# Optimization experiments

Measured on AMD Instinct MI355X. Metric: run time of the kernel, lower is better.

Reference implementation:

```python
import jax, jax.numpy as jnp
import numpy as np

B, S, D = 1, 2048, 3072
H, DH = 24, 128
ENC, NIP = 512, 64
COND = (512 // 8) * (512 // 8) * 16 // 64  # 1024 cond tokens per lora
RANK, ALPHA, LW, IP_SCALE = 16, 16.0, 1.0, 1.0
EPS = 1e-5


def _rms(x):
    return x * jax.lax.rsqrt(jnp.mean(x * x, axis=-1, keepdims=True) + EPS)


def _to_heads(x):
    b, s, _ = x.shape
    return x.reshape(b, s, H, DH).transpose(0, 2, 1, 3)  # [B,H,S,DH]


def _from_heads(x):
    b, h, s, d = x.shape
    return x.transpose(0, 2, 1, 3).reshape(b, s, h * d)


def _lora(x, dn, up):
    # token mask keeps only the cond block (number=0, n_loras=1 -> last COND tokens)
    y = ((x[:, -COND:, :] @ dn) @ up) * (ALPHA / RANK)
    z = jnp.zeros((x.shape[0], x.shape[1] - COND, up.shape[1]), x.dtype)
    return jnp.concatenate([z, y], axis=1)


def _sdpa(q, k, v, mask=None):
    s = jnp.einsum('bhqd,bhkd->bhqk', q, k) * (1.0 / np.sqrt(DH))
    if mask is not None:
        s = s + mask
    return jnp.einsum('bhqk,bhkd->bhqd', jax.nn.softmax(s, axis=-1), v)


def _forward(hidden_states, encoder_hidden_states, image_emb,
             Wq, bq, Wk, bk, Wv, bv, Waq, baq, Wak, bak, Wav, bav,
             Wo, bo, Wao, bao, Wkip, Wvip,
             lq_dn, lq_up, lk_dn, lk_up, lv_dn, lv_up, lp_dn, lp_up):
    hs, ehs, img = hidden_states, encoder_hidden_states, image_emb
    # context (encoder) projections + RMSNorm on q/k
    eq = _rms(_to_heads(ehs @ Waq + baq))
    ek = _rms(_to_heads(ehs @ Wak + bak))
    ev = _to_heads(ehs @ Wav + bav)
    # main-stream q/k/v with masked LoRA branches
    q = hs @ Wq + bq + LW * _lora(hs, lq_dn, lq_up)
    k = hs @ Wk + bk + LW * _lora(hs, lk_dn, lk_up)
    v = hs @ Wv + bv + LW * _lora(hs, lv_dn, lv_up)
    q = _rms(_to_heads(q))
    k = _rms(_to_heads(k))
    v = _to_heads(v)
    # IP-adapter branch: extra K/V from image_emb, norm_added_k is RMSNorm(128)
    kip = _rms(_to_heads(img @ Wkip))
    vip = _to_heads(img @ Wvip)
    ip_out = _from_heads(_sdpa(q, kip, vip))  # [B,S,D]
    # concat encoder stream ahead of main stream
    q = jnp.concatenate([eq, q], axis=2)
    k = jnp.concatenate([ek, k], axis=2)
    v = jnp.concatenate([ev, v], axis=2)
    SL = ENC + S
    SB = SL - COND  # scaled_block_size
    m = jnp.ones((SL, SL), jnp.float32)
    m = m.at[:SB, :].set(0.0)        # non-cond rows attend everywhere
    m = m.at[SB:, SB:].set(0.0)      # single cond block attends to itself (n_loras=1)
    mask = m * (-1e20)
    out = _from_heads(_sdpa(q, k, v, mask))  # [B,SL,D]
    enc_out = out[:, :ENC, :]
    main = out[:, ENC:, :] + IP_SCALE * ip_out
    main = main @ Wo + bo
    main = main + LW * _lora(main, lp_dn, lp_up)  # proj LoRA (to_out dropout=identity)
    enc_out = enc_out @ Wao + bao
    return jnp.concatenate([enc_out, main], axis=1)  # [B, ENC+S, D]


def setup_inputs():
    key = jax.random.key(0)
    ks = iter(jax.random.split(key, 40))
    w = lambda *sh: jax.random.normal(next(ks), sh, jnp.float32) * 0.02
    return dict(
        hidden_states=jax.random.normal(next(ks), (B, S, D), jnp.float32),
        encoder_hidden_states=jax.random.normal(next(ks), (B, ENC, D), jnp.float32),
        image_emb=jax.random.normal(next(ks), (B, NIP, D), jnp.float32),
        Wq=w(D, D), bq=w(D), Wk=w(D, D), bk=w(D), Wv=w(D, D), bv=w(D),
        Waq=w(D, D), baq=w(D), Wak=w(D, D), bak=w(D), Wav=w(D, D), bav=w(D),
        Wo=w(D, D), bo=w(D), Wao=w(D, D), bao=w(D),
        Wkip=w(D, D), Wvip=w(D, D),
        lq_dn=w(D, RANK), lq_up=w(RANK, D), lk_dn=w(D, RANK), lk_up=w(RANK, D),
        lv_dn=w(D, RANK), lv_up=w(RANK, D), lp_dn=w(D, RANK), lp_up=w(RANK, D),
    )


def reference(hidden_states, encoder_hidden_states, image_emb,
              Wq, bq, Wk, bk, Wv, bv, Waq, baq, Wak, bak, Wav, bav,
              Wo, bo, Wao, bao, Wkip, Wvip,
              lq_dn, lq_up, lk_dn, lk_up, lv_dn, lv_up, lp_dn, lp_up):
    return _forward(hidden_states, encoder_hidden_states, image_emb,
                    Wq, bq, Wk, bk, Wv, bv, Waq, baq, Wak, bak, Wav, bav,
                    Wo, bo, Wao, bao, Wkip, Wvip,
                    lq_dn, lq_up, lk_dn, lk_up, lv_dn, lv_up, lp_dn, lp_up)
```

## Files before the change

kernel.cpp:

```cpp
#include <hip/hip_runtime.h>

typedef unsigned short u16;
typedef short s16x8 __attribute__((ext_vector_type(8)));
typedef float f32x4 __attribute__((ext_vector_type(4)));
typedef const __attribute__((address_space(1))) unsigned int* as1_u32p;
typedef __attribute__((address_space(3))) unsigned int* as3_u32p;

static_assert(sizeof(s16x8) == 16, "");

struct alignas(8) U16x4 { u16 x, y, z, w; };

__device__ __forceinline__ u16 f2bf(float f) {
  union { float f; unsigned u; } c; c.f = f;
  return (u16)((c.u + 0x7fffu + ((c.u >> 16) & 1u)) >> 16);
}
__device__ __forceinline__ float bf2f(u16 h) {
  union { unsigned u; float f; } c; c.u = ((unsigned)h) << 16;
  return c.f;
}
__device__ __forceinline__ void async16(const void* g, void* l) {
  __builtin_amdgcn_global_load_lds((as1_u32p)g, (as3_u32p)l, 16, 0, 0);
}

__launch_bounds__(256)
__global__ void lora_dn3(const float* __restrict__ X, int ldx,
                         const float* __restrict__ d0, const float* __restrict__ d1,
                         const float* __restrict__ d2, float* __restrict__ t) {
  __shared__ float red[4][48];
  const int m = blockIdx.x;
  const float* xr = X + (long)m * ldx;
  float p[48];
#pragma unroll
  for (int r = 0; r < 48; ++r) p[r] = 0.f;
  for (int k = threadIdx.x; k < 3072; k += 256) {
    float a = xr[k];
    const float* e0 = d0 + (long)k * 16;
    const float* e1 = d1 + (long)k * 16;
    const float* e2 = d2 + (long)k * 16;
#pragma unroll
    for (int r = 0; r < 16; ++r) {
      p[r]      += a * e0[r];
      p[16 + r] += a * e1[r];
      p[32 + r] += a * e2[r];
    }
  }
#pragma unroll
  for (int r = 0; r < 48; ++r)
#pragma unroll
    for (int st = 1; st < 64; st <<= 1) p[r] += __shfl_xor(p[r], st, 64);
  int lane = threadIdx.x & 63, w = threadIdx.x >> 6;
  if (lane == 0) {
#pragma unroll
    for (int r = 0; r < 48; ++r) red[w][r] = p[r];
  }
  __syncthreads();
  if (threadIdx.x < 48) {
    int r = threadIdx.x;
    t[(long)m * 48 + r] = red[0][r] + red[1][r] + red[2][r] + red[3][r];
  }
}

__launch_bounds__(256)
__global__ void wod_prep(const float* __restrict__ Wo, const float* __restrict__ bo,
                         const float* __restrict__ dn, float* __restrict__ Wod) {
  __shared__ float red[4][16];
  const int m = blockIdx.x;
  const float* xr = (m < 3072) ? Wo + (long)m * 3072 : bo;
  float p[16];
#pragma unroll
  for (int r = 0; r < 16; ++r) p[r] = 0.f;
  for (int k = threadIdx.x; k < 3072; k += 256) {
    float a = xr[k];
    const float* d = dn + (long)k * 16;
#pragma unroll
    for (int r = 0; r < 16; ++r) p[r] += a * d[r];
  }
#pragma unroll
  for (int r = 0; r < 16; ++r)
#pragma unroll
    for (int st = 1; st < 64; st <<= 1) p[r] += __shfl_xor(p[r], st, 64);
  int lane = threadIdx.x & 63, w = threadIdx.x >> 6;
  if (lane == 0) {
#pragma unroll
    for (int r = 0; r < 16; ++r) red[w][r] = p[r];
  }
  __syncthreads();
  if (threadIdx.x < 16) {
    int r = threadIdx.x;
    Wod[(long)m * 16 + r] = red[0][r] + red[1][r] + red[2][r] + red[3][r];
  }
}

__launch_bounds__(256)
__global__ void prep_all(const float* __restrict__ hs, const float* __restrict__ tl,
                         u16* __restrict__ hsb,
                         const float* __restrict__ ehs, u16* __restrict__ ehsb,
                         const float* __restrict__ img, u16* __restrict__ imgb,
                         const float* __restrict__ baq, const float* __restrict__ bak,
                         const float* __restrict__ bav, const float* __restrict__ bq,
                         const float* __restrict__ bk, const float* __restrict__ bv,
                         float* __restrict__ bpk,
                         const float* __restrict__ u0, const float* __restrict__ u1,
                         const float* __restrict__ u2, u16* __restrict__ WTbM) {
  const int b = blockIdx.x;
  if (b < 3136) {
    long idx = (long)b * 256 + threadIdx.x;
    long m = idx / 392, c = idx % 392;
    U16x4 o0, o1;
    if (c < 384) {
      const float* p = hs + m * 3072 + c * 8;
      float4 a = *(const float4*)p;
      float4 bb = *(const float4*)(p + 4);
      o0 = U16x4{f2bf(a.x), f2bf(a.y), f2bf(a.z), f2bf(a.w)};
      o1 = U16x4{f2bf(bb.x), f2bf(bb.y), f2bf(bb.z), f2bf(bb.w)};
    } else {
      u16 t[8];
#pragma unroll
      for (int i = 0; i < 8; ++i) {
        int r = (int)(c - 384) * 8 + i;
        float v = (m >= 1024 && r < 48) ? tl[(m - 1024) * 48 + r] : 0.f;
        t[i] = f2bf(v);
      }
      o0 = U16x4{t[0], t[1], t[2], t[3]};
      o1 = U16x4{t[4], t[5], t[6], t[7]};
    }
    u16* d = hsb + m * 3136 + c * 8;
    *(U16x4*)d = o0;
    *(U16x4*)(d + 4) = o1;
  } else if (b < 3904) {
    long i = ((long)(b - 3136) * 256 + threadIdx.x) * 8;
    float4 a = *(const float4*)(ehs + i);
    float4 bb = *(const float4*)(ehs + i + 4);
    *(U16x4*)(ehsb + i) = U16x4{f2bf(a.x), f2bf(a.y), f2bf(a.z), f2bf(a.w)};
    *(U16x4*)(ehsb + i + 4) = U16x4{f2bf(bb.x), f2bf(bb.y), f2bf(bb.z), f2bf(bb.w)};
  } else if (b < 4000) {
    long i = ((long)(b - 3904) * 256 + threadIdx.x) * 8;
    float4 a = *(const float4*)(img + i);
    float4 bb = *(const float4*)(img + i + 4);
    *(U16x4*)(imgb + i) = U16x4{f2bf(a.x), f2bf(a.y), f2bf(a.z), f2bf(a.w)};
    *(U16x4*)(imgb + i + 4) = U16x4{f2bf(bb.x), f2bf(bb.y), f2bf(bb.z), f2bf(bb.w)};
  } else if (b < 4072) {
    int i = (b - 4000) * 256 + threadIdx.x;
    if (i < 9216)
      bpk[i] = (i < 3072) ? baq[i] : (i < 6144) ? bak[i - 3072] : bav[i - 6144];
    else {
      int j = i - 9216;
      bpk[i] = (j < 3072) ? bq[j] : (j < 6144) ? bk[j - 3072] : bv[j - 6144];
    }
  } else {
    int idx = (b - 4072) * 256 + threadIdx.x;
    int n = idx >> 6, i = idx & 63;
    int seg = n / 3072;
    const float* up = (seg == 0) ? u0 : (seg == 1) ? u1 : u2;
    int r = i - seg * 16;
    float v = (r >= 0 && r < 16) ? up[(long)r * 3072 + (n - seg * 3072)] : 0.f;
    WTbM[(long)n * 3136 + 3072 + i] = f2bf(v);
  }
}

struct WT6 { const float* src[6]; u16* dst[6]; int ldd[6]; };

__launch_bounds__(256)
__global__ void transpose_w(WT6 args) {
  const float* src = args.src[blockIdx.z];
  u16* dst = args.dst[blockIdx.z];
  const int ldd = args.ldd[blockIdx.z];
  __shared__ float tile[32][33];
  int k0 = blockIdx.x * 32, n0 = blockIdx.y * 32;
  int r = threadIdx.x >> 3, c4 = (threadIdx.x & 7) * 4;
  float4 v = *(const float4*)(src + (long)(k0 + r) * 3072 + n0 + c4);
  tile[r][c4 + 0] = v.x; tile[r][c4 + 1] = v.y;
  tile[r][c4 + 2] = v.z; tile[r][c4 + 3] = v.w;
  __syncthreads();
  U16x4 o{f2bf(tile[c4 + 0][r]), f2bf(tile[c4 + 1][r]),
          f2bf(tile[c4 + 2][r]), f2bf(tile[c4 + 3][r])};
  *(U16x4*)(dst + (long)(n0 + r) * ldd + k0 + c4) = o;
}

__launch_bounds__(256)
__global__ void fill_wo_tail(const float* __restrict__ lp_up, u16* __restrict__ WTbM) {
  int idx = blockIdx.x * 256 + threadIdx.x;
  int n = idx >> 6, i = idx & 63;
  float v = (i < 16) ? lp_up[(long)i * 3072 + n] : 0.f;
  WTbM[(long)n * 3136 + 3072 + i] = f2bf(v);
}

__launch_bounds__(256)
__global__ void t_tail(u16* __restrict__ At, const float* __restrict__ Wod) {
  __shared__ float red[4][16];
  const int tok = blockIdx.x;
  u16* tail = At + (long)(512 + tok) * 3136 + 3072;
  if (tok < 1024) {
    if (threadIdx.x < 64) tail[threadIdx.x] = 0;
    return;
  }
  const u16* xr = At + (long)(512 + tok) * 3136;
  float p[16];
#pragma unroll
  for (int r = 0; r < 16; ++r) p[r] = 0.f;
  for (int n = threadIdx.x; n < 3072; n += 256) {
    float a = bf2f(xr[n]);
    const float* wd = Wod + (long)n * 16;
#pragma unroll
    for (int r = 0; r < 16; ++r) p[r] += a * wd[r];
  }
#pragma unroll
  for (int r = 0; r < 16; ++r)
#pragma unroll
    for (int st = 1; st < 64; st <<= 1) p[r] += __shfl_xor(p[r], st, 64);
  int lane = threadIdx.x & 63, w = threadIdx.x >> 6;
  if (lane == 0) {
#pragma unroll
    for (int r = 0; r < 16; ++r) red[w][r] = p[r];
  }
  __syncthreads();
  if (threadIdx.x < 64) {
    if (threadIdx.x < 16) {
      int r = threadIdx.x;
      float t = red[0][r] + red[1][r] + red[2][r] + red[3][r] + Wod[3072L * 16 + r];
      tail[r] = f2bf(t);
    } else {
      tail[threadIdx.x] = 0;
    }
  }
}

template <int BM, int MI, int NI>
__launch_bounds__(256)
__global__ void gemm_f32(const u16* __restrict__ A, int lda,
                         const u16* __restrict__ B, int ldb,
                         float* __restrict__ C, int ldc,
                         const float* __restrict__ bias, int KC, long cstride) {
  constexpr int WCOLS = 128 / (NI * 16);
  constexpr int ABYTES = BM * 128;
  __shared__ char smem[ABYTES + 128 * 128];
  char* As = smem;
  char* Bs = smem + ABYTES;
// ... 58 lines not shown
    for (int ni = 0; ni < NI; ++ni) {
      long col = n0 + wc * (NI * 16) + ni * 16 + lr;
      float bv = bias ? bias[col] : 0.f;
#pragma unroll
      for (int j = 0; j < 4; ++j) {
        long row = m0 + wr * (MI * 16) + mi * 16 + lg * 4 + j;
        C[row * ldc + col] = acc[mi][ni][j] + bv;
      }
    }
  }
}

__launch_bounds__(256)
__global__ void rms_ip(const float* __restrict__ in, u16* __restrict__ Ko,
                       u16* __restrict__ Vo) {
  const int t = blockIdx.x & 63;
  const int vhalf = blockIdx.x >> 6;
  const int col0 = vhalf ? 3072 : 0;
  u16* out = vhalf ? Vo : Ko;
  const int w = threadIdx.x >> 6, lane = threadIdx.x & 63;
  const long ps = 64LL * 6144;
#pragma unroll
  for (int hh = 0; hh < 6; ++hh) {
    int h = w * 6 + hh;
    const float* x = in + (long)t * 6144 + col0 + h * 128 + lane * 2;
    float a = x[0] + x[ps] + x[2 * ps] + x[3 * ps];
    float b = x[1] + x[1 + ps] + x[1 + 2 * ps] + x[1 + 3 * ps];
    float scale = 1.f;
    if (!vhalf) {
      float ss = a * a + b * b;
#pragma unroll
      for (int st = 1; st < 64; st <<= 1) ss += __shfl_xor(ss, st, 64);
      scale = rsqrtf(ss * (1.f / 128.f) + 1e-5f);
    }
    unsigned pa = f2bf(a * scale), pb = f2bf(b * scale);
    *(unsigned*)(out + ((long)h * 64 + t) * 128 + lane * 2) = pa | (pb << 16);
  }
}

__launch_bounds__(256)
__global__ void transpose_v(const u16* __restrict__ VB, u16* __restrict__ VT, int T) {
  __shared__ u16 tile[32][34];
  int h = blockIdx.z;
  int t0 = blockIdx.x * 32, d0 = blockIdx.y * 32;
  int r = threadIdx.x >> 3, c4 = (threadIdx.x & 7) * 4;
  U16x4 v = *(const U16x4*)(VB + ((long)h * T + t0 + r) * 128 + d0 + c4);
  tile[r][c4 + 0] = v.x; tile[r][c4 + 1] = v.y;
  tile[r][c4 + 2] = v.z; tile[r][c4 + 3] = v.w;
  __syncthreads();
  U16x4 o{tile[c4 + 0][r], tile[c4 + 1][r], tile[c4 + 2][r], tile[c4 + 3][r]};
  *(U16x4*)(VT + ((long)h * 128 + d0 + r) * T + t0 + c4) = o;
}

__launch_bounds__(256, 2)
__global__ void gemm_qkv(const u16* __restrict__ Aenc, const u16* __restrict__ Amain,
                         const u16* __restrict__ Benc, const u16* __restrict__ Bmain,
                         u16* __restrict__ Qo, u16* __restrict__ Ko, u16* __restrict__ VTo,
                         const float* __restrict__ bpk) {
  __shared__ char smem[49152];
  char* As = smem;
  char* Bs = smem + 16384;
  const int tid = threadIdx.x;
  const int w = tid >> 6, lane = tid & 63;
  const int lr = lane & 15, lg = lane >> 4;
  const int wr = w >> 1, wc = w & 1;
  const int flat = blockIdx.y * 20 + blockIdx.x;
  const int swz = (flat & 7) * 90 + (flat >> 3);
  const int mx = swz % 20;
  const long n0 = (long)(swz / 20) * 256;
  const u16* A;
  const u16* B;
  const float* bias;
  int lda, ldb, K, t0;
  long m0;
  if (mx < 4) {
    A = Aenc; lda = 3072; B = Benc; ldb = 3072; K = 3072; t0 = 0;
    m0 = (long)mx * 128; bias = bpk;
  } else {
    A = Amain; lda = 3136; B = Bmain; ldb = 3136; K = 3136; t0 = 512;
    m0 = (long)(mx - 4) * 128; bias = bpk + 9216;
  }
  f32x4 acc[4][8] = {};
  for (int kb = 0; kb < K; kb += 64) {
    __syncthreads();
#pragma unroll
    for (int i = 0; i < 4; ++i) {
      int x = (tid + 256 * i) * 16;
      int row = x >> 7;
      int sx = (x & 127) ^ ((row & 7) << 4);
      async16((const char*)(A + (m0 + row) * lda + kb) + sx, As + x);
    }
#pragma unroll
    for (int i = 0; i < 8; ++i) {
      int x = (tid + 256 * i) * 16;
      int row = x >> 7;
      int sx = (x & 127) ^ ((row & 7) << 4);
      async16((const char*)(B + (n0 + row) * ldb + kb) + sx, Bs + x);
    }
    __syncthreads();
#pragma unroll
    for (int kc = 0; kc < 2; ++kc) {
      s16x8 af[4], bfr[8];
#pragma unroll
      for (int mi = 0; mi < 4; ++mi) {
        int row = wr * 64 + mi * 16 + lr;
        af[mi] = *(const s16x8*)(As + (row << 7) + ((kc * 64 + lg * 16) ^ ((row & 7) << 4)));
      }
#pragma unroll
      for (int ni = 0; ni < 8; ++ni) {
        int row = wc * 128 + ni * 16 + lr;
        bfr[ni] = *(const s16x8*)(Bs + (row << 7) + ((kc * 64 + lg * 16) ^ ((row & 7) << 4)));
      }
#pragma unroll
      for (int mi = 0; mi < 4; ++mi)
#pragma unroll
        for (int ni = 0; ni < 8; ++ni)
          acc[mi][ni] = __builtin_amdgcn_mfma_f32_16x16x32_bf16(af[mi], bfr[ni], acc[mi][ni], 0, 0, 0);
    }
  }
  const int seg = (int)(n0 / 3072);
  const int head0 = (int)((n0 % 3072) >> 7);
#pragma unroll
  for (int ni = 0; ni < 8; ++ni) {
    float bv = bias[n0 + wc * 128 + ni * 16 + lr];
#pragma unroll
    for (int mi = 0; mi < 4; ++mi)
#pragma unroll
      for (int j = 0; j < 4; ++j) acc[mi][ni][j] += bv;
  }
  float scl[4][4];
  if (seg < 2) {
#pragma unroll
    for (int mi = 0; mi < 4; ++mi)
#pragma unroll
      for (int j = 0; j < 4; ++j) {
        float s = 0.f;
#pragma unroll
        for (int ni = 0; ni < 8; ++ni) s += acc[mi][ni][j] * acc[mi][ni][j];
#pragma unroll
        for (int st = 1; st < 16; st <<= 1) s += __shfl_xor(s, st, 16);
        scl[mi][j] = rsqrtf(s * (1.f / 128.f) + 1e-5f);
      }
  }
#pragma unroll
  for (int ph = 0; ph < 2; ++ph) {
    __syncthreads();
    if (wc == ph) {
      if (seg < 2) {
#pragma unroll
        for (int mi = 0; mi < 4; ++mi)
#pragma unroll
          for (int ni = 0; ni < 8; ++ni) {
            int d2 = (ni * 16 + lr) * 2;
#pragma unroll
            for (int j = 0; j < 4; ++j) {
              int tok = wr * 64 + mi * 16 + lg * 4 + j;
              *(u16*)(smem + tok * 256 + (d2 ^ ((tok & 7) << 4))) =
                  f2bf(acc[mi][ni][j] * scl[mi][j]);
            }
          }
      } else {
#pragma unroll
        for (int mi = 0; mi < 4; ++mi)
#pragma unroll
          for (int ni = 0; ni < 8; ++ni) {
            int d = ni * 16 + lr;
            int tok0b = (wr * 64 + mi * 16 + lg * 4) * 2;
            U16x4 o{f2bf(acc[mi][ni][0]), f2bf(acc[mi][ni][1]),
                    f2bf(acc[mi][ni][2]), f2bf(acc[mi][ni][3])};
            *(U16x4*)(smem + d * 256 + (tok0b ^ ((d & 7) << 4))) = o;
          }
      }
    }
    __syncthreads();
    const int headp = head0 + ph;
#pragma unroll
    for (int i = 0; i < 8; ++i) {
      int x = (tid + 256 * i) * 16;
      int row = x >> 8, col = x & 255;
      s16x8 vdat = *(const s16x8*)(smem + row * 256 + (col ^ ((row & 7) << 4)));
      if (seg < 2) {
        u16* g = (seg == 0 ? Qo : Ko) + ((long)headp * 2560 + t0 + m0 + row) * 128;
        *(s16x8*)((char*)g + col) = vdat;
      } else {
        u16* g = VTo + ((long)headp * 128 + row) * 2560 + t0 + m0;
        *(s16x8*)((char*)g + col) = vdat;
      }
    }
  }
}

__launch_bounds__(256)
__global__ void gemm_out(const u16* __restrict__ Atok, const u16* __restrict__ Benc,
                         const u16* __restrict__ Bmain, float* __restrict__ outp,
                         const float* __restrict__ bao, const float* __restrict__ bo) {
  __shared__ char smem[128 * 128 + 128 * 128];
  char* As = smem;
  char* Bs = smem + 128 * 128;
  const int tid = threadIdx.x;
  const int w = tid >> 6, lane = tid & 63;
  const int lr = lane & 15, lg = lane >> 4;
  const int wr = w >> 1, wc = w & 1;
  const int flat = blockIdx.y * 20 + blockIdx.x;
  const int swz = (flat & 7) * 60 + (flat >> 3);
  const int mx = swz % 20;
  const long n0 = (long)(swz / 20) * 128;
  const u16* A;
  const u16* B;
  const float* bias;
  float* C;
  int ldb, K;
  long m0;
  if (mx < 4) {
    A = Atok; B = Benc; ldb = 3072; K = 3072; bias = bao; C = outp;
    m0 = (long)mx * 128;
  } else {
    A = Atok + 512L * 3136; B = Bmain; ldb = 3136; K = 3136; bias = bo;
    C = outp + 512L * 3072; m0 = (long)(mx - 4) * 128;
  }
  f32x4 acc[4][4] = {};
  for (int kb = 0; kb < K; kb += 64) {
    __syncthreads();
#pragma unroll
    for (int i = 0; i < 4; ++i) {
      int x = (tid + 256 * i) * 16;
      int row = x >> 7;
      int sx = x ^ ((row & 7) << 4);
      async16((const char*)(A + (m0 + row) * 3136 + kb) + (sx & 127),
              As + ((w << 10) + (i << 12)));
    }
#pragma unroll
    for (int i = 0; i < 4; ++i) {
      int x = (tid + 256 * i) * 16;
      int row = x >> 7;
      int sx = x ^ ((row & 7) << 4);
      async16((const char*)(B + (n0 + row) * ldb + kb) + (sx & 127),
              Bs + ((w << 10) + (i << 12)));
    }
    __syncthreads();
#pragma unroll
    for (int kc = 0; kc < 2; ++kc) {
      s16x8 af[4], bfr[4];
#pragma unroll
      for (int mi = 0; mi < 4; ++mi) {
        int row = wr * 64 + mi * 16 + lr;
        int b = ((row << 7) + kc * 64 + lg * 16) ^ ((row & 7) << 4);
        af[mi] = *(const s16x8*)(As + b);
      }
#pragma unroll
      for (int ni = 0; ni < 4; ++ni) {
        int row = wc * 64 + ni * 16 + lr;
        int b = ((row << 7) + kc * 64 + lg * 16) ^ ((row & 7) << 4);
        bfr[ni] = *(const s16x8*)(Bs + b);
      }
#pragma unroll
      for (int mi = 0; mi < 4; ++mi)
#pragma unroll
        for (int ni = 0; ni < 4; ++ni)
          acc[mi][ni] = __builtin_amdgcn_mfma_f32_16x16x32_bf16(af[mi], bfr[ni], acc[mi][ni], 0, 0, 0);
    }
  }
#pragma unroll
  for (int mi = 0; mi < 4; ++mi) {
#pragma unroll
    for (int ni = 0; ni < 4; ++ni) {
      long col = n0 + wc * 64 + ni * 16 + lr;
      float bv = bias[col];
#pragma unroll
      for (int j = 0; j < 4; ++j) {
        long row = m0 + wr * 64 + mi * 16 + lg * 4 + j;
        C[row * 3072 + col] = acc[mi][ni][j] + bv;
      }
    }
  }
}

__launch_bounds__(512, 4)
__global__ void attn_fused(const u16* __restrict__ QB, const u16* __restrict__ KB,
                           const u16* __restrict__ VT, const u16* __restrict__ KipB,
                           const u16* __restrict__ VipT, u16* __restrict__ OutTok) {
  __shared__ char smem[81920];
  const int tid = threadIdx.x, w = tid >> 6, lane = tid & 63;
  const int lr = lane & 15, lg = lane >> 4;
  const int h = blockIdx.y;
  const int q0 = blockIdx.x * 128;
  const bool ip = (q0 >= 512);
  const u16* Qrow = QB + (long)(h * 2560 + q0 + w * 16 + lr) * 128;
  s16x8 qf[4];
#pragma unroll
  for (int dc = 0; dc < 4; ++dc) qf[dc] = *(const s16x8*)(Qrow + dc * 32 + lg * 8);
  f32x4 accO[8] = {};
  float l_r[4] = {0.f, 0.f, 0.f, 0.f};
  const int kv0 = (q0 >= 1536) ? 1536 : 0;
  const float sc = 0.08838834764831845f;

  auto stage_main = [&](int kv, int buf) {
#pragma unroll
    for (int i = 0; i < 2; ++i) {
      int x = (tid + 512 * i) * 16;
      int row = x >> 8;
      int sx = x ^ ((row & 7) << 4);
      async16((const char*)(KB + (long)(h * 2560 + kv + row) * 128) + (sx & 255),
              smem + buf * 16384 + ((i << 13) + (w << 10)));
    }
#pragma unroll
    for (int i = 0; i < 2; ++i) {
      int x = (tid + 512 * i) * 16;
      int row = x >> 7;
      int sx = x ^ ((row & 7) << 4);
      async16((const char*)(VT + (long)(h * 128 + row) * 2560 + kv) + (sx & 127),
              smem + 32768 + buf * 16384 + ((i << 13) + (w << 10)));
    }
  };
  auto stage_ip = [&](int buf) {
#pragma unroll
    for (int i = 0; i < 2; ++i) {
      int x = (tid + 512 * i) * 16;
      int row = x >> 8;
      int sx = x ^ ((row & 7) << 4);
      async16((const char*)(KipB + (long)(h * 64 + row) * 128) + (sx & 255),
              smem + buf * 16384 + ((i << 13) + (w << 10)));
    }
#pragma unroll
    for (int i = 0; i < 2; ++i) {
      int x = (tid + 512 * i) * 16;
      int row = x >> 7;
      int sx = x ^ ((row & 7) << 4);
      async16((const char*)(VipT + (long)(h * 128 + row) * 64) + (sx & 127),
              smem + 32768 + buf * 16384 + ((i << 13) + (w << 10)));
    }
  };

  stage_main(kv0, 0);
  __syncthreads();
  int cur = 0;
  for (int kv = kv0; kv < 2560; kv += 64) {
    if (kv + 64 < 2560) stage_main(kv + 64, cur ^ 1);
    else if (ip) stage_ip(cur ^ 1);
    const char* Ks = smem + cur * 16384;
    const char* Vs = smem + 32768 + cur * 16384;
    char* Pw = smem + 65536 + w * 2048;
    f32x4 s[4] = {};
#pragma unroll
    for (int kt = 0; kt < 4; ++kt)
#pragma unroll
      for (int dc = 0; dc < 4; ++dc) {
        int row = kt * 16 + lr;
        int b = ((row << 8) + dc * 64 + lg * 16) ^ ((row & 7) << 4);
        s16x8 kf = *(const s16x8*)(Ks + b);
        s[kt] = __builtin_amdgcn_mfma_f32_16x16x32_bf16(qf[dc], kf, s[kt], 0, 0, 0);
      }
#pragma unroll
    for (int kt = 0; kt < 4; ++kt)
#pragma unroll
      for (int j = 0; j < 4; ++j) {
        float pv = __expf(fmaf(s[kt][j], sc, -12.0f));
        l_r[j] += pv;
        int prow = lg * 4 + j;
        int b = ((prow << 7) + (kt * 16 + lr) * 2) ^ ((prow & 7) << 4);
        *(u16*)(Pw + b) = f2bf(pv);
      }
    asm volatile("s_waitcnt lgkmcnt(0)" ::: "memory");
#pragma unroll
    for (int kc = 0; kc < 2; ++kc) {
      int pb = ((lr << 7) + kc * 64 + lg * 16) ^ ((lr & 7) << 4);
      s16x8 pf = *(const s16x8*)(Pw + pb);
#pragma unroll
      for (int dt = 0; dt < 8; ++dt) {
        int row = dt * 16 + lr;
        int b = ((row << 7) + kc * 64 + lg * 16) ^ ((row & 7) << 4);
        s16x8 vf = *(const s16x8*)(Vs + b);
        accO[dt] = __builtin_amdgcn_mfma_f32_16x16x32_bf16(pf, vf, accO[dt], 0, 0, 0);
      }
    }
    __syncthreads();
    cur ^= 1;
  }
#pragma unroll
  for (int j = 0; j < 4; ++j) {
#pragma unroll
    for (int st = 1; st < 16; st <<= 1) l_r[j] += __shfl_xor(l_r[j], st, 16);
    l_r[j] = 1.f / l_r[j];
  }
#pragma unroll
  for (int dt = 0; dt < 8; ++dt)
#pragma unroll
    for (int j = 0; j < 4; ++j) accO[dt][j] *= l_r[j];
  if (ip) {
    const char* Ks = smem + cur * 16384;
    const char* Vs = smem + 32768 + cur * 16384;
    char* Pw = smem + 65536 + w * 2048;
    f32x4 s2[4] = {};
#pragma unroll
    for (int kt = 0; kt < 4; ++kt)
#pragma unroll
      for (int dc = 0; dc < 4; ++dc) {
        int row = kt * 16 + lr;
        int b = ((row << 8) + dc * 64 + lg * 16) ^ ((row & 7) << 4);
        s16x8 kf = *(const s16x8*)(Ks + b);
        s2[kt] = __builtin_amdgcn_mfma_f32_16x16x32_bf16(qf[dc], kf, s2[kt], 0, 0, 0);
      }
    float p2[4][4];
    float l2[4] = {0.f, 0.f, 0.f, 0.f};
#pragma unroll
    for (int kt = 0; kt < 4; ++kt)
#pragma unroll
      for (int j = 0; j < 4; ++j) {
        float pv = __expf(fmaf(s2[kt][j], sc, -12.0f));
        p2[kt][j] = pv;
        l2[j] += pv;
      }
#pragma unroll
    for (int j = 0; j < 4; ++j) {
#pragma unroll
      for (int st = 1; st < 16; st <<= 1) l2[j] += __shfl_xor(l2[j], st, 16);
      l2[j] = 1.f / l2[j];
    }
#pragma unroll
    for (int kt = 0; kt < 4; ++kt)
#pragma unroll
      for (int j = 0; j < 4; ++j) {
        int prow = lg * 4 + j;
        int b = ((prow << 7) + (kt * 16 + lr) * 2) ^ ((prow & 7) << 4);
        *(u16*)(Pw + b) = f2bf(p2[kt][j] * l2[j]);
      }
    asm volatile("s_waitcnt lgkmcnt(0)" ::: "memory");
#pragma unroll
// ... 25 lines not shown
                              void* d_out, int out_size, void* d_ws, size_t ws_size,
                              hipStream_t stream) {
  const float* hs    = (const float*)d_in[0];
  const float* ehs   = (const float*)d_in[1];
  const float* img   = (const float*)d_in[2];
  const float* Wq    = (const float*)d_in[3];
  const float* bq    = (const float*)d_in[4];
  const float* Wk    = (const float*)d_in[5];
  const float* bk    = (const float*)d_in[6];
  const float* Wv    = (const float*)d_in[7];
  const float* bv    = (const float*)d_in[8];
  const float* Waq   = (const float*)d_in[9];
  const float* baq   = (const float*)d_in[10];
  const float* Wak   = (const float*)d_in[11];
  const float* bak   = (const float*)d_in[12];
  const float* Wav   = (const float*)d_in[13];
  const float* bav   = (const float*)d_in[14];
  const float* Wo    = (const float*)d_in[15];
  const float* bo    = (const float*)d_in[16];
  const float* Wao   = (const float*)d_in[17];
  const float* bao   = (const float*)d_in[18];
  const float* Wkip  = (const float*)d_in[19];
  const float* Wvip  = (const float*)d_in[20];
  const float* lq_dn = (const float*)d_in[21];
  const float* lq_up = (const float*)d_in[22];
  const float* lk_dn = (const float*)d_in[23];
  const float* lk_up = (const float*)d_in[24];
  const float* lv_dn = (const float*)d_in[25];
  const float* lv_up = (const float*)d_in[26];
  const float* lp_dn = (const float*)d_in[27];
  const float* lp_up = (const float*)d_in[28];
  float* outp = (float*)d_out;

  char* ws = (char*)d_ws;
  size_t off = 0;
  auto take = [&](size_t b) { char* p = ws + off; off += (b + 255) & ~(size_t)255; return p; };
  u16*   WTbE = (u16*)take(3LL * 3072 * 3072 * 2);
  u16*   WTbM = (u16*)take(3LL * 3072 * 3136 * 2);
  u16*   hsb  = (u16*)take(2048LL * 3136 * 2);
  u16*   ehsb = (u16*)take(512LL * 3072 * 2);
  u16*   imgb = (u16*)take(64LL * 3072 * 2);
  u16*   VTf  = (u16*)take(24LL * 128 * 2560 * 2);
  float* IP0  = (float*)take(4LL * 64 * 6144 * 4);
  u16*   KipB = (u16*)take(24LL * 64 * 128 * 2);
  u16*   VipB = (u16*)take(24LL * 64 * 128 * 2);
  u16*   VipT = (u16*)take(24LL * 128 * 64 * 2);
  float* bpk  = (float*)take(2 * 9216 * 4);
  float* tl   = (float*)take(1024LL * 48 * 4);
  float* Wod  = (float*)take(3073LL * 16 * 4);
  u16* QBf = (u16*)d_out;
  u16* KBf = (u16*)d_out + 24LL * 2560 * 128;
  u16* AttnTok = hsb;
  u16* E1 = WTbE + 3072LL * 3072;

  lora_dn3<<<1024, 256, 0, stream>>>(hs + 1024LL * 3072, 3072, lq_dn, lk_dn, lv_dn, tl);
  prep_all<<<6376, 256, 0, stream>>>(hs, tl, hsb, ehs, ehsb, img, imgb,
                                     baq, bak, bav, bq, bk, bv, bpk,
                                     lq_up, lk_up, lv_up, WTbM);
  wod_prep<<<3073, 256, 0, stream>>>(Wo, bo, lp_dn, Wod);

  {
    WT6 a;
    a.src[0] = Waq; a.dst[0] = WTbE;                    a.ldd[0] = 3072;
    a.src[1] = Wak; a.dst[1] = WTbE + 3072LL * 3072;    a.ldd[1] = 3072;
    a.src[2] = Wav; a.dst[2] = WTbE + 2 * 3072LL * 3072; a.ldd[2] = 3072;
    a.src[3] = Wq;  a.dst[3] = WTbM;                    a.ldd[3] = 3136;
    a.src[4] = Wk;  a.dst[4] = WTbM + 3072LL * 3136;    a.ldd[4] = 3136;
    a.src[5] = Wv;  a.dst[5] = WTbM + 2 * 3072LL * 3136; a.ldd[5] = 3136;
    transpose_w<<<dim3(96, 96, 6), 256, 0, stream>>>(a);
  }

  gemm_qkv<<<dim3(20, 36), 256, 0, stream>>>(ehsb, hsb, WTbE, WTbM, QBf, KBf, VTf, bpk);

  {
    WT6 a;
    a.src[0] = Wao;  a.dst[0] = WTbE;                    a.ldd[0] = 3072;
    a.src[1] = Wkip; a.dst[1] = E1;                      a.ldd[1] = 3072;
    a.src[2] = Wvip; a.dst[2] = WTbE + 2 * 3072LL * 3072; a.ldd[2] = 3072;
    a.src[3] = Wo;   a.dst[3] = WTbM;                    a.ldd[3] = 3136;
    a.src[4] = Wao;  a.dst[4] = WTbE;                    a.ldd[4] = 3072;
    a.src[5] = Wao;  a.dst[5] = WTbE;                    a.ldd[5] = 3072;
    transpose_w<<<dim3(96, 96, 4), 256, 0, stream>>>(a);
  }
  fill_wo_tail<<<768, 256, 0, stream>>>(lp_up, WTbM);

  gemm_f32<64, 4, 2><<<dim3(1, 48, 4), 256, 0, stream>>>(imgb, 3072, E1, 3072, IP0, 6144,
                                                          nullptr, 768, 64LL * 6144);
  rms_ip<<<128, 256, 0, stream>>>(IP0, KipB, VipB);
  transpose_v<<<dim3(2, 4, 24), 256, 0, stream>>>(VipB, VipT, 64);

  attn_fused<<<dim3(20, 24), 512, 0, stream>>>(QBf, KBf, VTf, KipB, VipT, AttnTok);

  t_tail<<<2048, 256, 0, stream>>>(AttnTok, Wod);
  gemm_out<<<dim3(20, 24), 256, 0, stream>>>(AttnTok, WTbE, WTbM, outp, bao, bo);
}
```

Before: 642.5 us.

## Merge prep kernels, shrink QKV GEMM tile, overlap Wo transposes with attention

Weight transposes, Wod preparation and the input casts now run in one large prep launch. The QKV GEMM tile shrinks from 128x256 to 128x128 with less shared memory and higher occupancy, so RMSNorm needs a cross-wave shared-memory reduction. The Wao/Wo transposes and the LoRA tail fill are folded into the attention launch as extra blocks so they can overlap with attention work. Attention blocks are reordered so the heavier ones are scheduled first, and setprio is added around the MFMA sections. The risks are more block-launch overhead, branch divergence in the merged kernels, and reduced attention occupancy from the launch-bounds change.

```diff
diff --git a/kernel.cpp b/kernel.cpp
--- a/kernel.cpp
+++ b/kernel.cpp
@@ -61,110 +61,132 @@
 }
 
 __launch_bounds__(256)
-__global__ void wod_prep(const float* __restrict__ Wo, const float* __restrict__ bo,
-                         const float* __restrict__ dn, float* __restrict__ Wod) {
-  __shared__ float red[4][16];
-  const int m = blockIdx.x;
-  const float* xr = (m < 3072) ? Wo + (long)m * 3072 : bo;
-  float p[16];
-#pragma unroll
-  for (int r = 0; r < 16; ++r) p[r] = 0.f;
-  for (int k = threadIdx.x; k < 3072; k += 256) {
-    float a = xr[k];
-    const float* d = dn + (long)k * 16;
-#pragma unroll
-    for (int r = 0; r < 16; ++r) p[r] += a * d[r];
-  }
-#pragma unroll
-  for (int r = 0; r < 16; ++r)
-#pragma unroll
-    for (int st = 1; st < 64; st <<= 1) p[r] += __shfl_xor(p[r], st, 64);
-  int lane = threadIdx.x & 63, w = threadIdx.x >> 6;
-  if (lane == 0) {
-#pragma unroll
-    for (int r = 0; r < 16; ++r) red[w][r] = p[r];
-  }
-  __syncthreads();
-  if (threadIdx.x < 16) {
-    int r = threadIdx.x;
-    Wod[(long)m * 16 + r] = red[0][r] + red[1][r] + red[2][r] + red[3][r];
-  }
-}
+__global__ void mega_prep(const float* __restrict__ Waq, const float* __restrict__ Wak,
+                          const float* __restrict__ Wav, const float* __restrict__ Wq,
+                          const float* __restrict__ Wk, const float* __restrict__ Wv,
+                          u16* __restrict__ WTbE, u16* __restrict__ WTbM,
+                          const float* __restrict__ Wo, const float* __restrict__ bo,
+                          const float* __restrict__ lp_dn, float* __restrict__ Wod,
+                          const float* __restrict__ hs, const float* __restrict__ tl,
+                          u16* __restrict__ hsb,
+                          const float* __restrict__ ehs, u16* __restrict__ ehsb,
+                          const float* __restrict__ img, u16* __restrict__ imgb,
+                          const float* __restrict__ baq, const float* __restrict__ bak,
+                          const float* __restrict__ bav, const float* __restrict__ bq,
+                          const float* __restrict__ bk, const float* __restrict__ bv,
+                          float* __restrict__ bpk,
+                          const float* __restrict__ u0, const float* __restrict__ u1,
+                          const float* __restrict__ u2) {
+  __shared__ char lmem[4352];
+  const int b = blockIdx.x;
+  if (b < 55296) {
+    int mat = b / 9216, tile = b % 9216;
+    const float* src = (mat == 0) ? Waq : (mat == 1) ? Wak : (mat == 2) ? Wav
+                       : (mat == 3) ? Wq : (mat == 4) ? Wk : Wv;
+    u16* dst = (mat < 3) ? WTbE + (long)mat * 3072 * 3072
+                         : WTbM + (long)(mat - 3) * 3072 * 3136;
+    const int ldd = (mat < 3) ? 3072 : 3136;
+    float (*tile2)[33] = (float(*)[33])lmem;
+    int k0 = (tile / 96) * 32, n0 = (tile % 96) * 32;
+    int r = threadIdx.x >> 3, c4 = (threadIdx.x & 7) * 4;
+    float4 v = *(const float4*)(src + (long)(k0 + r) * 3072 + n0 + c4);
+    tile2[r][c4 + 0] = v.x; tile2[r][c4 + 1] = v.y;
+    tile2[r][c4 + 2] = v.z; tile2[r][c4 + 3] = v.w;
+    __syncthreads();
+    U16x4 o{f2bf(tile2[c4 + 0][r]), f2bf(tile2[c4 + 1][r]),
+            f2bf(tile2[c4 + 2][r]), f2bf(tile2[c4 + 3][r])};
+    *(U16x4*)(dst + (long)(n0 + r) * ldd + k0 + c4) = o;
+  } else if (b < 58369) {
+    const int m = b - 55296;
+    float (*red)[16] = (float(*)[16])lmem;
+    const float* xr = (m < 3072) ? Wo + (long)m * 3072 : bo;
+    float p[16];
+#pragma unroll
+    for (int r = 0; r < 16; ++r) p[r] = 0.f;
+    for (int k = threadIdx.x; k < 3072; k += 256) {
+      float a = xr[k];
+      const float* d = lp_dn + (long)k * 16;
+#pragma unroll
+      for (int r = 0; r < 16; ++r) p[r] += a * d[r];
+    }
+#pragma unroll
+    for (int r = 0; r < 16; ++r)
+#pragma unroll
+      for (int st = 1; st < 64; st <<= 1) p[r] += __shfl_xor(p[r], st, 64);
+    int lane = threadIdx.x & 63, w = threadIdx.x >> 6;
+    if (lane == 0) {
+#pragma unroll
+      for (int r = 0; r < 16; ++r) red[w][r] = p[r];
+    }
+    __syncthreads();
+    if (threadIdx.x < 16) {
+      int r = threadIdx.x;
+      Wod[(long)m * 16 + r] = red[0][r] + red[1][r] + red[2][r] + red[3][r];
+    }
+  } else {
+    const int pb = b - 58369;
+    if (pb < 3136) {
+      long idx = (long)pb * 256 + threadIdx.x;
+      long m = idx / 392, c = idx % 392;
+      U16x4 o0, o1;
+      if (c < 384) {
+        const float* p = hs + m * 3072 + c * 8;
+        float4 a = *(const float4*)p;
+        float4 bb = *(const float4*)(p + 4);
+        o0 = U16x4{f2bf(a.x), f2bf(a.y), f2bf(a.z), f2bf(a.w)};
+        o1 = U16x4{f2bf(bb.x), f2bf(bb.y), f2bf(bb.z), f2bf(bb.w)};
+      } else {
+        u16 t[8];
+#pragma unroll
+        for (int i = 0; i < 8; ++i) {
+          int r = (int)(c - 384) * 8 + i;
+          float v = (m >= 1024 && r < 48) ? tl[(m - 1024) * 48 + r] : 0.f;
+          t[i] = f2bf(v);
+        }
+        o0 = U16x4{t[0], t[1], t[2], t[3]};
+        o1 = U16x4{t[4], t[5], t[6], t[7]};
+      }
+      u16* d = hsb + m * 3136 + c * 8;
+      *(U16x4*)d = o0;
+      *(U16x4*)(d + 4) = o1;
+    } else if (pb < 3904) {
+      long i = ((long)(pb - 3136) * 256 + threadIdx.x) * 8;
+      float4 a = *(const float4*)(ehs + i);
+      float4 bb = *(const float4*)(ehs + i + 4);
+      *(U16x4*)(ehsb + i) = U16x4{f2bf(a.x), f2bf(a.y), f2bf(a.z), f2bf(a.w)};
+      *(U16x4*)(ehsb + i + 4) = U16x4{f2bf(bb.x), f2bf(bb.y), f2bf(bb.z), f2bf(bb.w)};
+    } else if (pb < 4000) {
+      long i = ((long)(pb - 3904) * 256 + threadIdx.x) * 8;
+      float4 a = *(const float4*)(img + i);
+      float4 bb = *(const float4*)(img + i + 4);
+      *(U16x4*)(imgb + i) = U16x4{f2bf(a.x), f2bf(a.y), f2bf(a.z), f2bf(a.w)};
+      *(U16x4*)(imgb + i + 4) = U16x4{f2bf(bb.x), f2bf(bb.y), f2bf(bb.z), f2bf(bb.w)};
+    } else if (pb < 4072) {
+      int i = (pb - 4000) * 256 + threadIdx.x;
+      if (i < 9216)
+        bpk[i] = (i < 3072) ? baq[i] : (i < 6144) ? bak[i - 3072] : bav[i - 6144];
+      else {
+        int j = i - 9216;
+        bpk[i] = (j < 3072) ? bq[j] : (j < 6144) ? bk[j - 3072] : bv[j - 6144];
+      }
+    } else {
+      int idx = (pb - 4072) * 256 + threadIdx.x;
+      int n = idx >> 6, i = idx & 63;
+      int seg = n / 3072;
+      const float* up = (seg == 0) ? u0 : (seg == 1) ? u1 : u2;
+      int r = i - seg * 16;
+      float v = (r >= 0 && r < 16) ? up[(long)r * 3072 + (n - seg * 3072)] : 0.f;
+      WTbM[(long)n * 3136 + 3072 + i] = f2bf(v);
+    }
+  }
+}
+
+struct WT2 { const float* src[2]; u16* dst[2]; };
 
 __launch_bounds__(256)
-__global__ void prep_all(const float* __restrict__ hs, const float* __restrict__ tl,
-                         u16* __restrict__ hsb,
-                         const float* __restrict__ ehs, u16* __restrict__ ehsb,
-                         const float* __restrict__ img, u16* __restrict__ imgb,
-                         const float* __restrict__ baq, const float* __restrict__ bak,
-                         const float* __restrict__ bav, const float* __restrict__ bq,
-                         const float* __restrict__ bk, const float* __restrict__ bv,
-                         float* __restrict__ bpk,
-                         const float* __restrict__ u0, const float* __restrict__ u1,
-                         const float* __restrict__ u2, u16* __restrict__ WTbM) {
-  const int b = blockIdx.x;
-  if (b < 3136) {
-    long idx = (long)b * 256 + threadIdx.x;
-    long m = idx / 392, c = idx % 392;
-    U16x4 o0, o1;
-    if (c < 384) {
-      const float* p = hs + m * 3072 + c * 8;
-      float4 a = *(const float4*)p;
-      float4 bb = *(const float4*)(p + 4);
-      o0 = U16x4{f2bf(a.x), f2bf(a.y), f2bf(a.z), f2bf(a.w)};
-      o1 = U16x4{f2bf(bb.x), f2bf(bb.y), f2bf(bb.z), f2bf(bb.w)};
-    } else {
-      u16 t[8];
-#pragma unroll
-      for (int i = 0; i < 8; ++i) {
-        int r = (int)(c - 384) * 8 + i;
-        float v = (m >= 1024 && r < 48) ? tl[(m - 1024) * 48 + r] : 0.f;
-        t[i] = f2bf(v);
-      }
-      o0 = U16x4{t[0], t[1], t[2], t[3]};
-      o1 = U16x4{t[4], t[5], t[6], t[7]};
-    }
-    u16* d = hsb + m * 3136 + c * 8;
-    *(U16x4*)d = o0;
-    *(U16x4*)(d + 4) = o1;
-  } else if (b < 3904) {
-    long i = ((long)(b - 3136) * 256 + threadIdx.x) * 8;
-    float4 a = *(const float4*)(ehs + i);
-    float4 bb = *(const float4*)(ehs + i + 4);
-    *(U16x4*)(ehsb + i) = U16x4{f2bf(a.x), f2bf(a.y), f2bf(a.z), f2bf(a.w)};
-    *(U16x4*)(ehsb + i + 4) = U16x4{f2bf(bb.x), f2bf(bb.y), f2bf(bb.z), f2bf(bb.w)};
-  } else if (b < 4000) {
-    long i = ((long)(b - 3904) * 256 + threadIdx.x) * 8;
-    float4 a = *(const float4*)(img + i);
-    float4 bb = *(const float4*)(img + i + 4);
-    *(U16x4*)(imgb + i) = U16x4{f2bf(a.x), f2bf(a.y), f2bf(a.z), f2bf(a.w)};
-    *(U16x4*)(imgb + i + 4) = U16x4{f2bf(bb.x), f2bf(bb.y), f2bf(bb.z), f2bf(bb.w)};
-  } else if (b < 4072) {
-    int i = (b - 4000) * 256 + threadIdx.x;
-    if (i < 9216)
-      bpk[i] = (i < 3072) ? baq[i] : (i < 6144) ? bak[i - 3072] : bav[i - 6144];
-    else {
-      int j = i - 9216;
-      bpk[i] = (j < 3072) ? bq[j] : (j < 6144) ? bk[j - 3072] : bv[j - 6144];
-    }
-  } else {
-    int idx = (b - 4072) * 256 + threadIdx.x;
-    int n = idx >> 6, i = idx & 63;
-    int seg = n / 3072;
-    const float* up = (seg == 0) ? u0 : (seg == 1) ? u1 : u2;
-    int r = i - seg * 16;
-    float v = (r >= 0 && r < 16) ? up[(long)r * 3072 + (n - seg * 3072)] : 0.f;
-    WTbM[(long)n * 3136 + 3072 + i] = f2bf(v);
-  }
-}
-
-struct WT6 { const float* src[6]; u16* dst[6]; int ldd[6]; };
-
-__launch_bounds__(256)
-__global__ void transpose_w(WT6 args) {
+__global__ void transpose_kv(WT2 args) {
   const float* src = args.src[blockIdx.z];
   u16* dst = args.dst[blockIdx.z];
-  const int ldd = args.ldd[blockIdx.z];
   __shared__ float tile[32][33];
   int k0 = blockIdx.x * 32, n0 = blockIdx.y * 32;
   int r = threadIdx.x >> 3, c4 = (threadIdx.x & 7) * 4;
@@ -174,15 +196,7 @@
   __syncthreads();
   U16x4 o{f2bf(tile[c4 + 0][r]), f2bf(tile[c4 + 1][r]),
           f2bf(tile[c4 + 2][r]), f2bf(tile[c4 + 3][r])};
-  *(U16x4*)(dst + (long)(n0 + r) * ldd + k0 + c4) = o;
-}
-
-__launch_bounds__(256)
-__global__ void fill_wo_tail(const float* __restrict__ lp_up, u16* __restrict__ WTbM) {
-  int idx = blockIdx.x * 256 + threadIdx.x;
-  int n = idx >> 6, i = idx & 63;
-  float v = (i < 16) ? lp_up[(long)i * 3072 + n] : 0.f;
-  WTbM[(long)n * 3136 + 3072 + i] = f2bf(v);
+  *(U16x4*)(dst + (long)(n0 + r) * 3072 + k0 + c4) = o;
 }
 
 __launch_bounds__(256)
@@ -347,12 +361,12 @@
   *(U16x4*)(VT + ((long)h * 128 + d0 + r) * T + t0 + c4) = o;
 }
 
-__launch_bounds__(256, 2)
+__launch_bounds__(256, 3)
 __global__ void gemm_qkv(const u16* __restrict__ Aenc, const u16* __restrict__ Amain,
                          const u16* __restrict__ Benc, const u16* __restrict__ Bmain,
                          u16* __restrict__ Qo, u16* __restrict__ Ko, u16* __restrict__ VTo,
                          const float* __restrict__ bpk) {
-  __shared__ char smem[49152];
+  __shared__ char smem[32768];
   char* As = smem;
   char* Bs = smem + 16384;
   const int tid = threadIdx.x;
@@ -360,9 +374,9 @@
   const int lr = lane & 15, lg = lane >> 4;
   const int wr = w >> 1, wc = w & 1;
   const int flat = blockIdx.y * 20 + blockIdx.x;
-  const int swz = (flat & 7) * 90 + (flat >> 3);
+  const int swz = (flat & 7) * 180 + (flat >> 3);
   const int mx = swz % 20;
-  const long n0 = (long)(swz / 20) * 256;
+  const long n0 = (long)(swz / 20) * 128;
   const u16* A;
   const u16* B;
   const float* bias;
@@ -375,7 +389,7 @@
     A = Amain; lda = 3136; B = Bmain; ldb = 3136; K = 3136; t0 = 512;
     m0 = (long)(mx - 4) * 128; bias = bpk + 9216;
   }
-  f32x4 acc[4][8] = {};
+  f32x4 acc[4][4] = {};
   for (int kb = 0; kb < K; kb += 64) {
     __syncthreads();
 #pragma unroll
@@ -386,7 +400,7 @@
       async16((const char*)(A + (m0 + row) * lda + kb) + sx, As + x);
     }
 #pragma unroll
-    for (int i = 0; i < 8; ++i) {
+    for (int i = 0; i < 4; ++i) {
       int x = (tid + 256 * i) * 16;
       int row = x >> 7;
       int sx = (x & 127) ^ ((row & 7) << 4);
@@ -395,92 +409,98 @@
     __syncthreads();
 #pragma unroll
     for (int kc = 0; kc < 2; ++kc) {
-      s16x8 af[4], bfr[8];
+      s16x8 af[4], bfr[4];
 #pragma unroll
       for (int mi = 0; mi < 4; ++mi) {
         int row = wr * 64 + mi * 16 + lr;
         af[mi] = *(const s16x8*)(As + (row << 7) + ((kc * 64 + lg * 16) ^ ((row & 7) << 4)));
       }
 #pragma unroll
-      for (int ni = 0; ni < 8; ++ni) {
-        int row = wc * 128 + ni * 16 + lr;
+      for (int ni = 0; ni < 4; ++ni) {
+        int row = wc * 64 + ni * 16 + lr;
         bfr[ni] = *(const s16x8*)(Bs + (row << 7) + ((kc * 64 + lg * 16) ^ ((row & 7) << 4)));
       }
 #pragma unroll
       for (int mi = 0; mi < 4; ++mi)
 #pragma unroll
-        for (int ni = 0; ni < 8; ++ni)
+        for (int ni = 0; ni < 4; ++ni)
           acc[mi][ni] = __builtin_amdgcn_mfma_f32_16x16x32_bf16(af[mi], bfr[ni], acc[mi][ni], 0, 0, 0);
     }
   }
   const int seg = (int)(n0 / 3072);
-  const int head0 = (int)((n0 % 3072) >> 7);
-#pragma unroll
-  for (int ni = 0; ni < 8; ++ni) {
-    float bv = bias[n0 + wc * 128 + ni * 16 + lr];
+  const int head = (int)((n0 % 3072) >> 7);
+#pragma unroll
+  for (int ni = 0; ni < 4; ++ni) {
+    float bv = bias[n0 + wc * 64 + ni * 16 + lr];
 #pragma unroll
     for (int mi = 0; mi < 4; ++mi)
 #pragma unroll
       for (int j = 0; j < 4; ++j) acc[mi][ni][j] += bv;
   }
+  __syncthreads();
   float scl[4][4];
   if (seg < 2) {
+    float* red = (float*)smem;
 #pragma unroll
     for (int mi = 0; mi < 4; ++mi)
 #pragma unroll
       for (int j = 0; j < 4; ++j) {
         float s = 0.f;
 #pragma unroll
-        for (int ni = 0; ni < 8; ++ni) s += acc[mi][ni][j] * acc[mi][ni][j];
+        for (int ni = 0; ni < 4; ++ni) s += acc[mi][ni][j] * acc[mi][ni][j];
 #pragma unroll
         for (int st = 1; st < 16; st <<= 1) s += __shfl_xor(s, st, 16);
-        scl[mi][j] = rsqrtf(s * (1.f / 128.f) + 1e-5f);
-      }
-  }
-#pragma unroll
-  for (int ph = 0; ph < 2; ++ph) {
-    __syncthreads();
-    if (wc == ph) {
-      if (seg < 2) {
-#pragma unroll
-        for (int mi = 0; mi < 4; ++mi)
-#pragma unroll
-          for (int ni = 0; ni < 8; ++ni) {
-            int d2 = (ni * 16 + lr) * 2;
-#pragma unroll
-            for (int j = 0; j < 4; ++j) {
-              int tok = wr * 64 + mi * 16 + lg * 4 + j;
-              *(u16*)(smem + tok * 256 + (d2 ^ ((tok & 7) << 4))) =
-                  f2bf(acc[mi][ni][j] * scl[mi][j]);
-            }
-          }
-      } else {
-#pragma unroll
-        for (int mi = 0; mi < 4; ++mi)
-#pragma unroll
-          for (int ni = 0; ni < 8; ++ni) {
-            int d = ni * 16 + lr;
-            int tok0b = (wr * 64 + mi * 16 + lg * 4) * 2;
-            U16x4 o{f2bf(acc[mi][ni][0]), f2bf(acc[mi][ni][1]),
-                    f2bf(acc[mi][ni][2]), f2bf(acc[mi][ni][3])};
-            *(U16x4*)(smem + d * 256 + (tok0b ^ ((d & 7) << 4))) = o;
-          }
-      }
-    }
-    __syncthreads();
-    const int headp = head0 + ph;
-#pragma unroll
-    for (int i = 0; i < 8; ++i) {
-      int x = (tid + 256 * i) * 16;
-      int row = x >> 8, col = x & 255;
-      s16x8 vdat = *(const s16x8*)(smem + row * 256 + (col ^ ((row & 7) << 4)));
-      if (seg < 2) {
-        u16* g = (seg == 0 ? Qo : Ko) + ((long)headp * 2560 + t0 + m0 + row) * 128;
-        *(s16x8*)((char*)g + col) = vdat;
-      } else {
-        u16* g = VTo + ((long)headp * 128 + row) * 2560 + t0 + m0;
-        *(s16x8*)((char*)g + col) = vdat;
-      }
+        if (lr == 0) red[(wr * 64 + mi * 16 + lg * 4 + j) * 2 + wc] = s;
+        scl[mi][j] = s;
+      }
+    __syncthreads();
+#pragma unroll
+    for (int mi = 0; mi < 4; ++mi)
+#pragma unroll
+      for (int j = 0; j < 4; ++j) {
+        int row = wr * 64 + mi * 16 + lg * 4 + j;
+        float t = red[row * 2] + red[row * 2 + 1];
+        scl[mi][j] = rsqrtf(t * (1.f / 128.f) + 1e-5f);
+      }
+    __syncthreads();
+  }
+  if (seg < 2) {
+#pragma unroll
+    for (int mi = 0; mi < 4; ++mi)
+#pragma unroll
+      for (int ni = 0; ni < 4; ++ni) {
+        int d2 = (wc * 64 + ni * 16 + lr) * 2;
+#pragma unroll
+        for (int j = 0; j < 4; ++j) {
+          int tok = wr * 64 + mi * 16 + lg * 4 + j;
+          *(u16*)(smem + tok * 256 + (d2 ^ ((tok & 7) << 4))) =
+              f2bf(acc[mi][ni][j] * scl[mi][j]);
+        }
+      }
+  } else {
+#pragma unroll
+    for (int mi = 0; mi < 4; ++mi)
+#pragma unroll
+      for (int ni = 0; ni < 4; ++ni) {
+        int d = wc * 64 + ni * 16 + lr;
+        int tok0b = (wr * 64 + mi * 16 + lg * 4) * 2;
+        U16x4 o{f2bf(acc[mi][ni][0]), f2bf(acc[mi][ni][1]),
+                f2bf(acc[mi][ni][2]), f2bf(acc[mi][ni][3])};
+        *(U16x4*)(smem + d * 256 + (tok0b ^ ((d & 7) << 4))) = o;
+      }
+  }
+  __syncthreads();
+#pragma unroll
+  for (int i = 0; i < 8; ++i) {
+    int x = (tid + 256 * i) * 16;
+    int row = x >> 8, col = x & 255;
+    s16x8 vdat = *(const s16x8*)(smem + row * 256 + (col ^ ((row & 7) << 4)));
+    if (seg < 2) {
+      u16* g = (seg == 0 ? Qo : Ko) + ((long)head * 2560 + t0 + m0 + row) * 128;
+      *(s16x8*)((char*)g + col) = vdat;
+    } else {
+      u16* g = VTo + ((long)head * 128 + row) * 2560 + t0 + m0;
+      *(s16x8*)((char*)g + col) = vdat;
     }
   }
 }
@@ -570,15 +590,48 @@
   }
 }
 
-__launch_bounds__(512, 4)
-__global__ void attn_fused(const u16* __restrict__ QB, const u16* __restrict__ KB,
-                           const u16* __restrict__ VT, const u16* __restrict__ KipB,
-                           const u16* __restrict__ VipT, u16* __restrict__ OutTok) {
+__launch_bounds__(512, 2)
+__global__ void attn_mega(const u16* __restrict__ QB, const u16* __restrict__ KB,
+                          const u16* __restrict__ VT, const u16* __restrict__ KipB,
+                          const u16* __restrict__ VipT, u16* __restrict__ OutTok,
+                          const float* __restrict__ Wao, const float* __restrict__ Wo,
+                          u16* __restrict__ WTbE, u16* __restrict__ WTbM,
+                          const float* __restrict__ lp_up) {
   __shared__ char smem[81920];
-  const int tid = threadIdx.x, w = tid >> 6, lane = tid & 63;
+  const int bf = blockIdx.x;
+  const int tid = threadIdx.x;
+  if (bf >= 480) {
+    if (bf < 9696) {
+      int t2 = (bf - 480) * 2 + (tid >> 8);
+      int mat = t2 / 9216, tile = t2 % 9216;
+      const float* src = mat ? Wo : Wao;
+      u16* dst = mat ? WTbM : WTbE;
+      const int ldd = mat ? 3136 : 3072;
+      float (*tl2)[32][33] = (float(*)[32][33])smem;
+      int half = tid >> 8, lt = tid & 255;
+      int k0 = (tile / 96) * 32, n0t = (tile % 96) * 32;
+      int r = lt >> 3, c4 = (lt & 7) * 4;
+      float4 v = *(const float4*)(src + (long)(k0 + r) * 3072 + n0t + c4);
+      tl2[half][r][c4 + 0] = v.x; tl2[half][r][c4 + 1] = v.y;
+      tl2[half][r][c4 + 2] = v.z; tl2[half][r][c4 + 3] = v.w;
+      __syncthreads();
+      U16x4 o{f2bf(tl2[half][c4 + 0][r]), f2bf(tl2[half][c4 + 1][r]),
+              f2bf(tl2[half][c4 + 2][r]), f2bf(tl2[half][c4 + 3][r])};
+      *(U16x4*)(dst + (long)(n0t + r) * ldd + k0 + c4) = o;
+    } else {
+      int idx = (bf - 9696) * 512 + tid;
+      int n = idx >> 6, i = idx & 63;
+      float v = (i < 16) ? lp_up[(long)i * 3072 + n] : 0.f;
+      WTbM[(long)n * 3136 + 3072 + i] = f2bf(v);
+    }
+    return;
+  }
+  const int w = tid >> 6, lane = tid & 63;
   const int lr = lane & 15, lg = lane >> 4;
-  const int h = blockIdx.y;
-  const int q0 = blockIdx.x * 128;
+  int h, qb;
+  if (bf < 288) { h = bf / 12; qb = bf % 12; }
+  else { int s = bf - 288; h = s / 8; qb = 12 + s % 8; }
+  const int q0 = qb * 128;
   const bool ip = (q0 >= 512);
   const u16* Qrow = QB + (long)(h * 2560 + q0 + w * 16 + lr) * 128;
   s16x8 qf[4];
@@ -636,6 +689,7 @@
     const char* Vs = smem + 32768 + cur * 16384;
     char* Pw = smem + 65536 + w * 2048;
     f32x4 s[4] = {};
+    __builtin_amdgcn_s_setprio(1);
 #pragma unroll
     for (int kt = 0; kt < 4; ++kt)
 #pragma unroll
@@ -645,6 +699,7 @@
         s16x8 kf = *(const s16x8*)(Ks + b);
         s[kt] = __builtin_amdgcn_mfma_f32_16x16x32_bf16(qf[dc], kf, s[kt], 0, 0, 0);
       }
+    __builtin_amdgcn_s_setprio(0);
 #pragma unroll
     for (int kt = 0; kt < 4; ++kt)
 #pragma unroll
@@ -656,6 +711,7 @@
         *(u16*)(Pw + b) = f2bf(pv);
       }
     asm volatile("s_waitcnt lgkmcnt(0)" ::: "memory");
+    __builtin_amdgcn_s_setprio(1);
 #pragma unroll
     for (int kc = 0; kc < 2; ++kc) {
       int pb = ((lr << 7) + kc * 64 + lg * 16) ^ ((lr & 7) << 4);
@@ -668,6 +724,7 @@
         accO[dt] = __builtin_amdgcn_mfma_f32_16x16x32_bf16(pf, vf, accO[dt], 0, 0, 0);
       }
     }
+    __builtin_amdgcn_s_setprio(0);
     __syncthreads();
     cur ^= 1;
   }
@@ -799,44 +856,30 @@
   u16* KBf = (u16*)d_out + 24LL * 2560 * 128;
   u16* AttnTok = hsb;
   u16* E1 = WTbE + 3072LL * 3072;
+  u16* E2 = WTbE + 2 * 3072LL * 3072;
 
   lora_dn3<<<1024, 256, 0, stream>>>(hs + 1024LL * 3072, 3072, lq_dn, lk_dn, lv_dn, tl);
-  prep_all<<<6376, 256, 0, stream>>>(hs, tl, hsb, ehs, ehsb, img, imgb,
-                                     baq, bak, bav, bq, bk, bv, bpk,
-                                     lq_up, lk_up, lv_up, WTbM);
-  wod_prep<<<3073, 256, 0, stream>>>(Wo, bo, lp_dn, Wod);
+  mega_prep<<<64745, 256, 0, stream>>>(Waq, Wak, Wav, Wq, Wk, Wv, WTbE, WTbM,
+                                       Wo, bo, lp_dn, Wod,
+                                       hs, tl, hsb, ehs, ehsb, img, imgb,
+                                       baq, bak, bav, bq, bk, bv, bpk,
+                                       lq_up, lk_up, lv_up);
+
+  gemm_qkv<<<dim3(20, 72), 256, 0, stream>>>(ehsb, hsb, WTbE, WTbM, QBf, KBf, VTf, bpk);
 
   {
-    WT6 a;
-    a.src[0] = Waq; a.dst[0] = WTbE;                    a.ldd[0] = 3072;
-    a.src[1] = Wak; a.dst[1] = WTbE + 3072LL * 3072;    a.ldd[1] = 3072;
-    a.src[2] = Wav; a.dst[2] = WTbE + 2 * 3072LL * 3072; a.ldd[2] = 3072;
-    a.src[3] = Wq;  a.dst[3] = WTbM;                    a.ldd[3] = 3136;
-    a.src[4] = Wk;  a.dst[4] = WTbM + 3072LL * 3136;    a.ldd[4] = 3136;
-    a.src[5] = Wv;  a.dst[5] = WTbM + 2 * 3072LL * 3136; a.ldd[5] = 3136;
-    transpose_w<<<dim3(96, 96, 6), 256, 0, stream>>>(a);
-  }
-
-  gemm_qkv<<<dim3(20, 36), 256, 0, stream>>>(ehsb, hsb, WTbE, WTbM, QBf, KBf, VTf, bpk);
-
-  {
-    WT6 a;
-    a.src[0] = Wao;  a.dst[0] = WTbE;                    a.ldd[0] = 3072;
-    a.src[1] = Wkip; a.dst[1] = E1;                      a.ldd[1] = 3072;
-    a.src[2] = Wvip; a.dst[2] = WTbE + 2 * 3072LL * 3072; a.ldd[2] = 3072;
-    a.src[3] = Wo;   a.dst[3] = WTbM;                    a.ldd[3] = 3136;
-    a.src[4] = Wao;  a.dst[4] = WTbE;                    a.ldd[4] = 3072;
-    a.src[5] = Wao;  a.dst[5] = WTbE;                    a.ldd[5] = 3072;
-    transpose_w<<<dim3(96, 96, 4), 256, 0, stream>>>(a);
-  }
-  fill_wo_tail<<<768, 256, 0, stream>>>(lp_up, WTbM);
-
+    WT2 a;
+    a.src[0] = Wkip; a.dst[0] = E1;
+    a.src[1] = Wvip; a.dst[1] = E2;
+    transpose_kv<<<dim3(96, 96, 2), 256, 0, stream>>>(a);
+  }
   gemm_f32<64, 4, 2><<<dim3(1, 48, 4), 256, 0, stream>>>(imgb, 3072, E1, 3072, IP0, 6144,
                                                           nullptr, 768, 64LL * 6144);
   rms_ip<<<128, 256, 0, stream>>>(IP0, KipB, VipB);
   transpose_v<<<dim3(2, 4, 24), 256, 0, stream>>>(VipB, VipT, 64);
 
-  attn_fused<<<dim3(20, 24), 512, 0, stream>>>(QBf, KBf, VTf, KipB, VipT, AttnTok);
+  attn_mega<<<10080, 512, 0, stream>>>(QBf, KBf, VTf, KipB, VipT, AttnTok,
+                                       Wao, Wo, WTbE, WTbM, lp_up);
 
   t_tail<<<2048, 256, 0, stream>>>(AttnTok, Wod);
   gemm_out<<<dim3(20, 24), 256, 0, stream>>>(AttnTok, WTbE, WTbM, outp, bao, bo);
```

Result: faster. 577.2 us (-10.2%).
